# Kernel tuning notes

Measured on AMD Instinct MI355X. Metric: run time of the kernel, lower is better.

Reference implementation:

```python
import jax, jax.numpy as jnp
import numpy as np


def setup_inputs() -> dict:
    key = jax.random.key(0)
    k1, k2 = jax.random.split(key)
    x = jax.random.normal(k1, (64, 64, 32, 32), dtype=jnp.float32)
    codebook = jax.random.normal(k2, (1024, 64), dtype=jnp.float32)
    return {"x": x, "codebook": codebook}


def reference(x, codebook):
    B, C, H, W = x.shape
    # NCHW -> NHWC -> [N, C] flat tokens
    xt = jnp.transpose(x, (0, 2, 3, 1)).reshape(-1, C)  # [N, C]
    # squared euclidean distances [N, K] (argmin of squared == argmin of cdist)
    x_sq = jnp.sum(xt * xt, axis=-1, keepdims=True)          # [N, 1]
    cb_sq = jnp.sum(codebook * codebook, axis=-1)            # [K]
    d2 = x_sq - 2.0 * (xt @ codebook.T) + cb_sq[None, :]     # [N, K]
    idx_emb = jnp.argmin(d2, axis=-1)                        # [N]
    quant = codebook[idx_emb]                                # [N, C]
    loss_embed = jnp.mean((jax.lax.stop_gradient(xt) - quant) ** 2)
    loss_commitment = jnp.mean((xt - jax.lax.stop_gradient(quant)) ** 2)
    # straight-through estimator
    quant_out = xt + jax.lax.stop_gradient(quant - xt)
    quant_out = quant_out.reshape(B, H, W, C).transpose(0, 3, 1, 2)
    idx_emb = idx_emb.reshape(B, H * W)
    return quant_out, loss_embed, loss_commitment, idx_emb
```

## Files before the change

### kernel.cpp

```cpp
#include <hip/hip_runtime.h>

#define C_DIM 64
#define K_CODES 1024

#define QUANT_OFF 0
#define LOSS_OFF  4194304
#define IDX_OFF   4194306

#define WS_CBSQH_F 16
#define WS_STREAM_B 8192
#define SEG_BYTES 1024
#define CHUNK_BYTES 12288
#define N_CHUNKS 32
#define WS_NEEDED (WS_STREAM_B + N_CHUNKS * CHUNK_BYTES)

typedef float floatx16 __attribute__((ext_vector_type(16)));
typedef short bf16x8  __attribute__((ext_vector_type(8)));

typedef __attribute__((address_space(1))) const void gv_t;
typedef __attribute__((address_space(3))) void lv_t;

static __device__ inline unsigned short f2bf(float v) {
    unsigned int u = __float_as_uint(v);
    unsigned int r = (u + 0x7FFF + ((u >> 16) & 1)) >> 16;
    return (unsigned short)r;
}
static __device__ inline float bf2f(unsigned short b) {
    return __uint_as_float(((unsigned int)b) << 16);
}

__global__ void vq_prep(const float* __restrict__ cb, float* __restrict__ ws)
{
    const int tid = threadIdx.x;
    const int blk = blockIdx.x;
    if (blk >= 384) {
        int code = (blk - 384) * 64 + tid;
        const float4* row = reinterpret_cast<const float4*>(cb + code * C_DIM);
        float s = 0.f;
        #pragma unroll
        for (int j = 0; j < 16; ++j) {
            float4 v = row[j];
            s = fmaf(v.x, v.x, s); s = fmaf(v.y, v.y, s);
            s = fmaf(v.z, v.z, s); s = fmaf(v.w, v.w, s);
        }
        ws[WS_CBSQH_F + code] = 0.5f * s;
        return;
    }
    const int chunk = blk / 12;
    const int seg   = blk - chunk * 12;
    const int tb = seg >> 2;
    const int s4 = seg & 3;
    const int code = chunk * 32 + (tid & 31);
    const int c0   = s4 * 16 + ((tid >> 5) << 3);
    const float* src = cb + code * C_DIM + c0;
    unsigned short us[8];
    #pragma unroll
    for (int j = 0; j < 8; ++j) {
        float v  = src[j];
        float h  = bf2f(f2bf(v));
        float r1 = v - h;
        float m  = bf2f(f2bf(r1));
        float r2 = r1 - m;
        float sel = (tb == 0) ? h : (tb == 1) ? m : r2;
        us[j] = f2bf(-sel);
    }
    uint4 o;
    o.x = (unsigned)us[0] | ((unsigned)us[1] << 16);
    o.y = (unsigned)us[2] | ((unsigned)us[3] << 16);
    o.z = (unsigned)us[4] | ((unsigned)us[5] << 16);
    o.w = (unsigned)us[6] | ((unsigned)us[7] << 16);
    *reinterpret_cast<uint4*>((char*)ws + WS_STREAM_B + chunk * CHUNK_BYTES
                              + seg * SEG_BYTES + tid * 16) = o;
}

__global__ __launch_bounds__(512, 4) void vq_main(
    const float* __restrict__ x,
    const float* __restrict__ cb,
    const float* __restrict__ ws_f,
    float* __restrict__ out,
    double* __restrict__ ws_sum)
{
    __shared__ __align__(16) char smem[49152];
    __shared__ float cbsqh_s[K_CODES];
    __shared__ float redv[2][128];
    __shared__ int   redi[2][128];
    __shared__ int   kidx_s[128];

    const int tid  = threadIdx.x;
    const int tok0 = blockIdx.x * 128;
    const int b    = tok0 >> 10;
    const int hw0  = tok0 & 1023;

    const int w   = tid >> 6;
    const int ln  = tid & 63;
    const int tw  = w >> 1;
    const int kw  = w & 1;
    const int l31 = ln & 31;
    const int l5  = ln >> 5;

    float* xs = reinterpret_cast<float*>(smem);
    #pragma unroll
    for (int j = 0; j < 16; ++j) {
        int idx = j * 512 + tid;
        int c = idx >> 7, t = idx & 127;
        xs[c * 130 + t] = x[((b * C_DIM + c) << 10) + hw0 + t];
    }
    cbsqh_s[tid]       = ws_f[WS_CBSQH_F + tid];
    cbsqh_s[tid + 512] = ws_f[WS_CBSQH_F + tid + 512];
    __syncthreads();

    bf16x8 tf[3][4];
    {
        const int token = tw * 32 + l31;
        #pragma unroll
        for (int s4 = 0; s4 < 4; ++s4) {
            const int cb0 = s4 * 16 + l5 * 8;
            #pragma unroll
            for (int j = 0; j < 8; ++j) {
                float v  = xs[(cb0 + j) * 130 + token];
                float h  = bf2f(f2bf(v));
                float r1 = v - h;
                float m  = bf2f(f2bf(r1));
                float r2 = r1 - m;
                tf[0][s4][j] = (short)f2bf(h);
                tf[1][s4][j] = (short)f2bf(m);
                tf[2][s4][j] = (short)f2bf(r2);
            }
        }
    }
    __syncthreads();

    const char* stream = (const char*)ws_f + WS_STREAM_B;

    #pragma unroll
    for (int it = 0; it < 3; ++it) {
        int s  = w * 3 + it;
        int p  = s / 12;
        int si = s - p * 12;
        const char* g = stream + p * CHUNK_BYTES + si * SEG_BYTES + ln * 16;
        __builtin_amdgcn_global_load_lds((gv_t*)g,
            (lv_t*)(smem + p * 24576 + si * SEG_BYTES + ln * 16), 16, 0, 0);
    }
    __syncthreads();

    float minv = 3.4e38f;
    int   mini = 0;

    #pragma unroll 1
    for (int i = 0; i < 16; ++i) {
        if (i < 15) {
            #pragma unroll
            for (int it = 0; it < 3; ++it) {
                int s  = w * 3 + it;
                int p  = s / 12;
                int si = s - p * 12;
                const char* g = stream + (2 * (i + 1) + p) * CHUNK_BYTES + si * SEG_BYTES + ln * 16;
                __builtin_amdgcn_global_load_lds((gv_t*)g,
                    (lv_t*)(smem + p * 24576 + ((i + 1) & 1) * CHUNK_BYTES + si * SEG_BYTES + ln * 16),
                    16, 0, 0);
            }
        }

        const char* abase = smem + kw * 24576 + (i & 1) * CHUNK_BYTES;
        floatx16 accA, accB;
        #pragma unroll
        for (int r = 0; r < 16; ++r) { accA[r] = 0.f; accB[r] = 0.f; }

        #pragma unroll
        for (int tb = 0; tb < 3; ++tb) {
            #pragma unroll
            for (int s4 = 0; s4 < 4; ++s4) {
                bf16x8 as = *reinterpret_cast<const bf16x8*>(
                    abase + (tb * 4 + s4) * SEG_BYTES + ln * 16);
                #pragma unroll
                for (int a = 0; a < 3; ++a) {
                    if (a + tb <= 2) {
                        if (((a + s4) & 1) == 0)
                            accA = __builtin_amdgcn_mfma_f32_32x32x16_bf16(as, tf[a][s4], accA, 0, 0, 0);
                        else
                            accB = __builtin_amdgcn_mfma_f32_32x32x16_bf16(as, tf[a][s4], accB, 0, 0, 0);
                    }
                }
            }
        }

        const int chbase = (2 * i + kw) * 32;
        const float* cp = &cbsqh_s[chbase + 4 * l5];
        float4 cq0 = *reinterpret_cast<const float4*>(cp);
        float4 cq1 = *reinterpret_cast<const float4*>(cp + 8);
        float4 cq2 = *reinterpret_cast<const float4*>(cp + 16);
        float4 cq3 = *reinterpret_cast<const float4*>(cp + 24);
        float cqa[16] = {cq0.x, cq0.y, cq0.z, cq0.w, cq1.x, cq1.y, cq1.z, cq1.w,
                         cq2.x, cq2.y, cq2.z, cq2.w, cq3.x, cq3.y, cq3.z, cq3.w};
        #pragma unroll
        for (int r = 0; r < 16; ++r) {
            float v = accA[r] + accB[r] + cqa[r];
            int idx = chbase + 8 * (r >> 2) + 4 * l5 + (r & 3);
            if (v < minv) { minv = v; mini = idx; }
        }

        __syncthreads();
    }

    {
        float ov = __shfl_xor(minv, 32, 64);
        int   oi = __shfl_xor(mini, 32, 64);
        if (ov < minv || (ov == minv && oi < mini)) { minv = ov; mini = oi; }
        if (ln < 32) {
            redv[kw][tw * 32 + ln] = minv;
            redi[kw][tw * 32 + ln] = mini;
        }
    }
    __syncthreads();

    if (tid < 128) {
        float v0 = redv[0][tid]; int i0 = redi[0][tid];
        float v1 = redv[1][tid]; int i1 = redi[1][tid];
        int bi = (v1 < v0 || (v1 == v0 && i1 < i0)) ? i1 : i0;
        kidx_s[tid] = bi;
        out[IDX_OFF + tok0 + tid] = (float)bi;
    }
    __syncthreads();

    {
        const int i  = tid & 127;
        const int c0 = tid >> 7;
        const int kk = kidx_s[i];
        const float* crow = cb + kk * C_DIM;
        float lsum = 0.f;
        #pragma unroll
        for (int j = 0; j < 16; ++j) {
            int c = c0 * 16 + j;
            float q  = crow[c];
            float xv = x[((b * C_DIM + c) << 10) + hw0 + i];
            float d  = q - xv;
            lsum = fmaf(d, d, lsum);
            out[QUANT_OFF + ((b * C_DIM + c) << 10) + hw0 + i] = xv + d;
        }
        #pragma unroll
        for (int off = 32; off > 0; off >>= 1)
            lsum += __shfl_down(lsum, off, 64);
        if ((tid & 63) == 0)
            atomicAdd(ws_sum, (double)lsum);
    }
}

#define CB_PAD 68
__global__ __launch_bounds__(256, 2) void vq_main_valu(
    const float* __restrict__ x,
    const float* __restrict__ cb,
    float* __restrict__ out,
    double* __restrict__ ws_sum)
{
    __shared__ float xt_s[C_DIM][128];
    __shared__ float cb_s[C_DIM][CB_PAD];
    __shared__ float cbsq_all[K_CODES];
    __shared__ float red_v[8][128];
    __shared__ int   red_i[8][128];
    __shared__ int   kidx_s[128];

    const int tid  = threadIdx.x;
    const int tok0 = blockIdx.x * 128;
    const int b_img = tok0 >> 10;
    const int hw0   = tok0 & 1023;

    #pragma unroll
    for (int r = 0; r < 4; ++r) {
        int k = tid + r * 256;
        const float4* row = reinterpret_cast<const float4*>(cb + k * C_DIM);
        float s = 0.f;
        #pragma unroll
        for (int j = 0; j < 16; ++j) {
            float4 v = row[j];
            s = fmaf(v.x, v.x, s); s = fmaf(v.y, v.y, s);
            s = fmaf(v.z, v.z, s); s = fmaf(v.w, v.w, s);
        }
        cbsq_all[k] = s;
    }
    {
        const int i  = tid & 127;
        const int c0 = tid >> 7;
        #pragma unroll
        for (int j = 0; j < 32; ++j) {
            int c = c0 + 2 * j;
            xt_s[c][i] = x[((b_img * C_DIM + c) << 10) + hw0 + i];
        }
    }

    const int tl = tid & 31;
    const int kg = tid >> 5;
    float minv[4]; int mini[4];
    #pragma unroll
    for (int m = 0; m < 4; ++m) { minv[m] = 3.4e38f; mini[m] = 0; }

    for (int ch = 0; ch < 16; ++ch) {
        __syncthreads();
        for (int t = tid; t < 64 * C_DIM; t += 256) {
            int kl = t >> 6, c = t & 63;
            cb_s[c][kl] = cb[(ch * 64 + kl) * C_DIM + c];
        }
        __syncthreads();
        float dot[4][8];
        #pragma unroll
        for (int m = 0; m < 4; ++m)
            #pragma unroll
            for (int k = 0; k < 8; ++k) dot[m][k] = 0.f;
        #pragma unroll 4
        for (int c = 0; c < C_DIM; ++c) {
            float4 xv  = *reinterpret_cast<const float4*>(&xt_s[c][tl * 4]);
            float4 cv0 = *reinterpret_cast<const float4*>(&cb_s[c][kg * 8]);
            float4 cv1 = *reinterpret_cast<const float4*>(&cb_s[c][kg * 8 + 4]);
            float xa[4] = {xv.x, xv.y, xv.z, xv.w};
            float ca[8] = {cv0.x, cv0.y, cv0.z, cv0.w, cv1.x, cv1.y, cv1.z, cv1.w};
            #pragma unroll
            for (int m = 0; m < 4; ++m)
                #pragma unroll
                for (int k = 0; k < 8; ++k)
                    dot[m][k] = fmaf(xa[m], ca[k], dot[m][k]);
        }
        const int codebase = ch * 64 + kg * 8;
        #pragma unroll
        for (int k = 0; k < 8; ++k) {
            float csq = cbsq_all[codebase + k];
            #pragma unroll
            for (int m = 0; m < 4; ++m) {
                float sc = fmaf(-2.f, dot[m][k], csq);
                if (sc < minv[m]) { minv[m] = sc; mini[m] = codebase + k; }
            }
        }
    }
    #pragma unroll
    for (int m = 0; m < 4; ++m) {
        red_v[kg][tl * 4 + m] = minv[m];
        red_i[kg][tl * 4 + m] = mini[m];
    }
    __syncthreads();
    if (tid < 128) {
        float bv = red_v[0][tid]; int bi = red_i[0][tid];
        #pragma unroll
        for (int g = 1; g < 8; ++g) {
            float v = red_v[g][tid]; int ii = red_i[g][tid];
            if (v < bv || (v == bv && ii < bi)) { bv = v; bi = ii; }
        }
        kidx_s[tid] = bi;
        out[IDX_OFF + tok0 + tid] = (float)bi;
    }
    __syncthreads();
    {
        const int i  = tid & 127;
        const int c0 = tid >> 7;
        const int kk = kidx_s[i];
        const float* crow = cb + kk * C_DIM;
        float lsum = 0.f;
        #pragma unroll
        for (int j = 0; j < 32; ++j) {
            int c = c0 * 32 + j;
            float q  = crow[c];
            float xv = xt_s[c][i];
            float d  = q - xv;
            lsum = fmaf(d, d, lsum);
            out[QUANT_OFF + ((b_img * C_DIM + c) << 10) + hw0 + i] = xv + d;
        }
        #pragma unroll
        for (int off = 32; off > 0; off >>= 1)
            lsum += __shfl_down(lsum, off, 64);
        if ((tid & 63) == 0)
            atomicAdd(ws_sum, (double)lsum);
    }
}

__global__ void vq_finalize(const double* __restrict__ ws_sum,
                            float* __restrict__ out)
{
    float m = (float)(ws_sum[0] / 4194304.0);
    out[LOSS_OFF]     = m;
    out[LOSS_OFF + 1] = m;
}

extern "C" void kernel_launch(void* const* d_in, const int* in_sizes, int n_in,
                              void* d_out, int out_size, void* d_ws, size_t ws_size,
                              hipStream_t stream) {
    const float* x  = (const float*)d_in[0];
    const float* cb = (const float*)d_in[1];
    float* out      = (float*)d_out;

    hipMemsetAsync(d_ws, 0, sizeof(double), stream);
    if (ws_size >= (size_t)WS_NEEDED) {
        vq_prep<<<400, 64, 0, stream>>>(cb, (float*)d_ws);
        vq_main<<<512, 512, 0, stream>>>(x, cb, (const float*)d_ws, out, (double*)d_ws);
    } else {
        vq_main_valu<<<512, 256, 0, stream>>>(x, cb, out, (double*)d_ws);
    }
    vq_finalize<<<1, 1, 0, stream>>>((const double*)d_ws, out);
}
```

Before: 160.0 us.

## Switch split-precision distance GEMM from 3-way bf16 to 2-way fp16 MFMA

Replaces the three-term bf16 split (six MFMAs per segment) with a two-term fp16 hi/lo split needing three MFMAs per segment, and folds the codebook-norm bias into the accumulator init. The codebook stream shrinks, so each iteration now covers four 32-code chunks in a 64KB double-buffered LDS area over 8 iterations. Smaller changes vectorize the x tile load, spread the loss atomics over 8 double slots, and zero them inside the prep kernel in place of a memset. fp16 has less exponent range than bf16, so the argmin could change for inputs with very large or tiny magnitudes, and the bigger LDS footprint may reduce occupancy.

```diff
diff --git a/kernel.cpp b/kernel.cpp
--- a/kernel.cpp
+++ b/kernel.cpp
@@ -10,31 +10,28 @@
 #define WS_CBSQH_F 16
 #define WS_STREAM_B 8192
 #define SEG_BYTES 1024
-#define CHUNK_BYTES 12288
+#define CHUNK_BYTES 8192
 #define N_CHUNKS 32
 #define WS_NEEDED (WS_STREAM_B + N_CHUNKS * CHUNK_BYTES)
 
 typedef float floatx16 __attribute__((ext_vector_type(16)));
-typedef short bf16x8  __attribute__((ext_vector_type(8)));
+typedef _Float16 fp16x8 __attribute__((ext_vector_type(8)));
 
 typedef __attribute__((address_space(1))) const void gv_t;
 typedef __attribute__((address_space(3))) void lv_t;
 
-static __device__ inline unsigned short f2bf(float v) {
-    unsigned int u = __float_as_uint(v);
-    unsigned int r = (u + 0x7FFF + ((u >> 16) & 1)) >> 16;
-    return (unsigned short)r;
-}
-static __device__ inline float bf2f(unsigned short b) {
-    return __uint_as_float(((unsigned int)b) << 16);
+static __device__ inline unsigned short h2u(_Float16 h) {
+    union { _Float16 f; unsigned short u; } c; c.f = h; return c.u;
 }
 
 __global__ void vq_prep(const float* __restrict__ cb, float* __restrict__ ws)
 {
     const int tid = threadIdx.x;
     const int blk = blockIdx.x;
-    if (blk >= 384) {
-        int code = (blk - 384) * 64 + tid;
+    if (blk >= 256) {
+        if (blk == 271 && tid < 8)
+            reinterpret_cast<double*>(ws)[tid] = 0.0;
+        int code = (blk - 256) * 64 + tid;
         const float4* row = reinterpret_cast<const float4*>(cb + code * C_DIM);
         float s = 0.f;
         #pragma unroll
@@ -46,8 +43,8 @@
         ws[WS_CBSQH_F + code] = 0.5f * s;
         return;
     }
-    const int chunk = blk / 12;
-    const int seg   = blk - chunk * 12;
+    const int chunk = blk >> 3;
+    const int seg   = blk & 7;
     const int tb = seg >> 2;
     const int s4 = seg & 3;
     const int code = chunk * 32 + (tid & 31);
@@ -56,13 +53,11 @@
     unsigned short us[8];
     #pragma unroll
     for (int j = 0; j < 8; ++j) {
-        float v  = src[j];
-        float h  = bf2f(f2bf(v));
-        float r1 = v - h;
-        float m  = bf2f(f2bf(r1));
-        float r2 = r1 - m;
-        float sel = (tb == 0) ? h : (tb == 1) ? m : r2;
-        us[j] = f2bf(-sel);
+        float v = src[j];
+        _Float16 h = (_Float16)v;
+        float r = v - (float)h;
+        _Float16 sel = (tb == 0) ? (_Float16)(-v) : (_Float16)(-r);
+        us[j] = h2u(sel);
     }
     uint4 o;
     o.x = (unsigned)us[0] | ((unsigned)us[1] << 16);
@@ -80,7 +75,7 @@
     float* __restrict__ out,
     double* __restrict__ ws_sum)
 {
-    __shared__ __align__(16) char smem[49152];
+    __shared__ __align__(16) char smem[65536];
     __shared__ float cbsqh_s[K_CODES];
     __shared__ float redv[2][128];
     __shared__ int   redi[2][128];
@@ -100,16 +95,18 @@
 
     float* xs = reinterpret_cast<float*>(smem);
     #pragma unroll
-    for (int j = 0; j < 16; ++j) {
+    for (int j = 0; j < 4; ++j) {
         int idx = j * 512 + tid;
-        int c = idx >> 7, t = idx & 127;
-        xs[c * 130 + t] = x[((b * C_DIM + c) << 10) + hw0 + t];
+        int c   = idx >> 5;
+        int t4  = (idx & 31) << 2;
+        float4 v = *reinterpret_cast<const float4*>(&x[((b * C_DIM + c) << 10) + hw0 + t4]);
+        *reinterpret_cast<float4*>(&xs[c * 132 + t4]) = v;
     }
     cbsqh_s[tid]       = ws_f[WS_CBSQH_F + tid];
     cbsqh_s[tid + 512] = ws_f[WS_CBSQH_F + tid + 512];
     __syncthreads();
 
-    bf16x8 tf[3][4];
+    fp16x8 tf[2][4];
     {
         const int token = tw * 32 + l31;
         #pragma unroll
@@ -117,14 +114,11 @@
             const int cb0 = s4 * 16 + l5 * 8;
             #pragma unroll
             for (int j = 0; j < 8; ++j) {
-                float v  = xs[(cb0 + j) * 130 + token];
-                float h  = bf2f(f2bf(v));
-                float r1 = v - h;
-                float m  = bf2f(f2bf(r1));
-                float r2 = r1 - m;
-                tf[0][s4][j] = (short)f2bf(h);
-                tf[1][s4][j] = (short)f2bf(m);
-                tf[2][s4][j] = (short)f2bf(r2);
+                float v = xs[(cb0 + j) * 132 + token];
+                _Float16 h = (_Float16)v;
+                float r = v - (float)h;
+                tf[0][s4][j] = h;
+                tf[1][s4][j] = (_Float16)r;
             }
         }
     }
@@ -133,13 +127,13 @@
     const char* stream = (const char*)ws_f + WS_STREAM_B;
 
     #pragma unroll
-    for (int it = 0; it < 3; ++it) {
-        int s  = w * 3 + it;
-        int p  = s / 12;
-        int si = s - p * 12;
-        const char* g = stream + p * CHUNK_BYTES + si * SEG_BYTES + ln * 16;
+    for (int it = 0; it < 4; ++it) {
+        int s  = w * 4 + it;
+        int cl = s >> 3;
+        int si = s & 7;
+        const char* g = stream + cl * CHUNK_BYTES + si * SEG_BYTES + ln * 16;
         __builtin_amdgcn_global_load_lds((gv_t*)g,
-            (lv_t*)(smem + p * 24576 + si * SEG_BYTES + ln * 16), 16, 0, 0);
+            (lv_t*)(smem + cl * CHUNK_BYTES + si * SEG_BYTES + ln * 16), 16, 0, 0);
     }
     __syncthreads();
 
@@ -147,56 +141,54 @@
     int   mini = 0;
 
     #pragma unroll 1
-    for (int i = 0; i < 16; ++i) {
-        if (i < 15) {
-            #pragma unroll
-            for (int it = 0; it < 3; ++it) {
-                int s  = w * 3 + it;
-                int p  = s / 12;
-                int si = s - p * 12;
-                const char* g = stream + (2 * (i + 1) + p) * CHUNK_BYTES + si * SEG_BYTES + ln * 16;
+    for (int i = 0; i < 8; ++i) {
+        if (i < 7) {
+            #pragma unroll
+            for (int it = 0; it < 4; ++it) {
+                int s  = w * 4 + it;
+                int cl = s >> 3;
+                int si = s & 7;
+                const char* g = stream + (4 * (i + 1) + cl) * CHUNK_BYTES + si * SEG_BYTES + ln * 16;
                 __builtin_amdgcn_global_load_lds((gv_t*)g,
-                    (lv_t*)(smem + p * 24576 + ((i + 1) & 1) * CHUNK_BYTES + si * SEG_BYTES + ln * 16),
+                    (lv_t*)(smem + (((i + 1) & 1) * 32768) + cl * CHUNK_BYTES + si * SEG_BYTES + ln * 16),
                     16, 0, 0);
             }
         }
 
-        const char* abase = smem + kw * 24576 + (i & 1) * CHUNK_BYTES;
-        floatx16 accA, accB;
-        #pragma unroll
-        for (int r = 0; r < 16; ++r) { accA[r] = 0.f; accB[r] = 0.f; }
-
-        #pragma unroll
-        for (int tb = 0; tb < 3; ++tb) {
+        #pragma unroll
+        for (int sub = 0; sub < 2; ++sub) {
+            const int cl = 2 * kw + sub;
+            const char* abase = smem + (i & 1) * 32768 + cl * CHUNK_BYTES;
+            const int chbase = (4 * i + cl) * 32;
+
+            const float* cp = &cbsqh_s[chbase + 4 * l5];
+            float4 cq0 = *reinterpret_cast<const float4*>(cp);
+            float4 cq1 = *reinterpret_cast<const float4*>(cp + 8);
+            float4 cq2 = *reinterpret_cast<const float4*>(cp + 16);
+            float4 cq3 = *reinterpret_cast<const float4*>(cp + 24);
+            floatx16 p0, p1, p2;
+            p0[0] = cq0.x; p0[1] = cq0.y; p0[2]  = cq0.z; p0[3]  = cq0.w;
+            p0[4] = cq1.x; p0[5] = cq1.y; p0[6]  = cq1.z; p0[7]  = cq1.w;
+            p0[8] = cq2.x; p0[9] = cq2.y; p0[10] = cq2.z; p0[11] = cq2.w;
+            p0[12] = cq3.x; p0[13] = cq3.y; p0[14] = cq3.z; p0[15] = cq3.w;
+            #pragma unroll
+            for (int r = 0; r < 16; ++r) { p1[r] = 0.f; p2[r] = 0.f; }
+
             #pragma unroll
             for (int s4 = 0; s4 < 4; ++s4) {
-                bf16x8 as = *reinterpret_cast<const bf16x8*>(
-                    abase + (tb * 4 + s4) * SEG_BYTES + ln * 16);
-                #pragma unroll
-                for (int a = 0; a < 3; ++a) {
-                    if (a + tb <= 2) {
-                        if (((a + s4) & 1) == 0)
-                            accA = __builtin_amdgcn_mfma_f32_32x32x16_bf16(as, tf[a][s4], accA, 0, 0, 0);
-                        else
-                            accB = __builtin_amdgcn_mfma_f32_32x32x16_bf16(as, tf[a][s4], accB, 0, 0, 0);
-                    }
-                }
-            }
-        }
-
-        const int chbase = (2 * i + kw) * 32;
-        const float* cp = &cbsqh_s[chbase + 4 * l5];
-        float4 cq0 = *reinterpret_cast<const float4*>(cp);
-        float4 cq1 = *reinterpret_cast<const float4*>(cp + 8);
-        float4 cq2 = *reinterpret_cast<const float4*>(cp + 16);
-        float4 cq3 = *reinterpret_cast<const float4*>(cp + 24);
-        float cqa[16] = {cq0.x, cq0.y, cq0.z, cq0.w, cq1.x, cq1.y, cq1.z, cq1.w,
-                         cq2.x, cq2.y, cq2.z, cq2.w, cq3.x, cq3.y, cq3.z, cq3.w};
-        #pragma unroll
-        for (int r = 0; r < 16; ++r) {
-            float v = accA[r] + accB[r] + cqa[r];
-            int idx = chbase + 8 * (r >> 2) + 4 * l5 + (r & 3);
-            if (v < minv) { minv = v; mini = idx; }
+                fp16x8 a0 = *reinterpret_cast<const fp16x8*>(abase + (0 * 4 + s4) * SEG_BYTES + ln * 16);
+                fp16x8 a1 = *reinterpret_cast<const fp16x8*>(abase + (1 * 4 + s4) * SEG_BYTES + ln * 16);
+                p0 = __builtin_amdgcn_mfma_f32_32x32x16_f16(a0, tf[0][s4], p0, 0, 0, 0);
+                p1 = __builtin_amdgcn_mfma_f32_32x32x16_f16(a0, tf[1][s4], p1, 0, 0, 0);
+                p2 = __builtin_amdgcn_mfma_f32_32x32x16_f16(a1, tf[0][s4], p2, 0, 0, 0);
+            }
+
+            #pragma unroll
+            for (int r = 0; r < 16; ++r) {
+                float v = (p0[r] + p1[r]) + p2[r];
+                int idx = chbase + 8 * (r >> 2) + 4 * l5 + (r & 3);
+                if (v < minv) { minv = v; mini = idx; }
+            }
         }
 
         __syncthreads();
@@ -241,7 +233,7 @@
         for (int off = 32; off > 0; off >>= 1)
             lsum += __shfl_down(lsum, off, 64);
         if ((tid & 63) == 0)
-            atomicAdd(ws_sum, (double)lsum);
+            atomicAdd(&ws_sum[blockIdx.x & 7], (double)lsum);
     }
 }
 
@@ -365,16 +357,24 @@
         for (int off = 32; off > 0; off >>= 1)
             lsum += __shfl_down(lsum, off, 64);
         if ((tid & 63) == 0)
-            atomicAdd(ws_sum, (double)lsum);
+            atomicAdd(&ws_sum[blockIdx.x & 7], (double)lsum);
     }
 }
 
 __global__ void vq_finalize(const double* __restrict__ ws_sum,
                             float* __restrict__ out)
 {
-    float m = (float)(ws_sum[0] / 4194304.0);
+    double s = 0.0;
+    #pragma unroll
+    for (int j = 0; j < 8; ++j) s += ws_sum[j];
+    float m = (float)(s / 4194304.0);
     out[LOSS_OFF]     = m;
     out[LOSS_OFF + 1] = m;
+}
+
+__global__ void vq_zero8(double* __restrict__ ws_sum)
+{
+    if (threadIdx.x < 8) ws_sum[threadIdx.x] = 0.0;
 }
 
 extern "C" void kernel_launch(void* const* d_in, const int* in_sizes, int n_in,
@@ -384,11 +384,11 @@
     const float* cb = (const float*)d_in[1];
     float* out      = (float*)d_out;
 
-    hipMemsetAsync(d_ws, 0, sizeof(double), stream);
     if (ws_size >= (size_t)WS_NEEDED) {
-        vq_prep<<<400, 64, 0, stream>>>(cb, (float*)d_ws);
+        vq_prep<<<272, 64, 0, stream>>>(cb, (float*)d_ws);
         vq_main<<<512, 512, 0, stream>>>(x, cb, (const float*)d_ws, out, (double*)d_ws);
     } else {
+        vq_zero8<<<1, 64, 0, stream>>>((double*)d_ws);
         vq_main_valu<<<512, 256, 0, stream>>>(x, cb, out, (double*)d_ws);
     }
     vq_finalize<<<1, 1, 0, stream>>>((const double*)d_ws, out);
```

Result: faster. 140.6 us (-12.1%).
